# Performance work log

Measured on AMD Instinct MI355X. Metric: run time of the kernel, lower is better.

The kernel has to match this reference:

```python
import jax, jax.numpy as jnp
import numpy as np

IMAGE_SIZE = 256
VIEW_ANGLE = 30.0 * np.pi / 180.0  # NMR default viewing angle
SIGMA = 1e-2                        # softness of the differentiable coverage test
EPS = 1e-6


def setup_inputs() -> dict:
    key = jax.random.key(0)
    k1, k2, k3 = jax.random.split(key, 3)
    V, F = 502, 1000
    # normalize_vertices -> points on/near the unit sphere centered at origin
    verts = jax.random.normal(k1, (1, V, 3), dtype=jnp.float32)
    verts = verts / (jnp.linalg.norm(verts, axis=-1, keepdims=True) + EPS)
    faces = jax.random.randint(k2, (1, F, 3), 0, V, dtype=jnp.int32)
    camera_position = jnp.array([6.0, 10.0, -14.0], dtype=jnp.float32)
    # binary silhouette reference, as produced by (image.max(-1) > 0.1)
    image_ref = (jax.random.uniform(k3, (1, IMAGE_SIZE, IMAGE_SIZE)) > 0.5).astype(jnp.float32)
    return {"vertices": verts, "faces": faces, "camera_position": camera_position, "image_ref": image_ref}


def _look_at(vertices, eye):
    # camera_mode='look_at': at=origin, up=+y
    at = jnp.zeros(3, dtype=vertices.dtype)
    up = jnp.array([0.0, 1.0, 0.0], dtype=vertices.dtype)
    z = at - eye
    z = z / (jnp.linalg.norm(z) + EPS)
    x = jnp.cross(up, z)
    x = x / (jnp.linalg.norm(x) + EPS)
    y = jnp.cross(z, x)
    R = jnp.stack([x, y, z], axis=0)           # [3,3], rows are camera axes
    return jnp.einsum('bvj,ij->bvi', vertices - eye, R)  # [1,V,3]


def _render_silhouette(vertices, faces, eye):
    H = W = IMAGE_SIZE
    v = _look_at(vertices, eye)                # [1,V,3] camera space
    w = jnp.tan(jnp.asarray(VIEW_ANGLE, v.dtype))
    zc = v[..., 2]
    proj = jnp.stack([v[..., 0] / (zc * w), v[..., 1] / (zc * w)], axis=-1)  # [1,V,2] NDC xy
    fv = proj[0][faces[0]]                     # [F,3,2] projected triangle vertices
    v0, v1, v2 = fv[:, 0], fv[:, 1], fv[:, 2]

    # pixel centers in NDC, row 0 at top (y=+)
    xs = (2.0 * jnp.arange(W, dtype=v.dtype) + 1.0) / W - 1.0
    ys = 1.0 - (2.0 * jnp.arange(H, dtype=v.dtype) + 1.0) / H
    px = jnp.stack(jnp.meshgrid(xs, ys, indexing='xy'), axis=-1).reshape(-1, 2)  # [P,2]

    def edge_sdist(a, b):
        # signed distance of every pixel to line a->b, computed as px @ n^T - (a.n)
        e = b - a                                           # [F,2]
        n = jnp.stack([-e[:, 1], e[:, 0]], axis=-1)
        n = n / (jnp.linalg.norm(e, axis=-1, keepdims=True) + EPS)
        return px @ n.T - jnp.sum(a * n, axis=-1)[None, :]  # [P,F]

    # orient consistently via signed triangle area
    e01, e02 = v1 - v0, v2 - v0
    area = e01[:, 0] * e02[:, 1] - e01[:, 1] * e02[:, 0]    # [F]
    s = jnp.sign(area)[None, :]

    inv_sigma = 1.0 / SIGMA
    frag = (jax.nn.sigmoid(edge_sdist(v0, v1) * s * inv_sigma)
            * jax.nn.sigmoid(edge_sdist(v1, v2) * s * inv_sigma)
            * jax.nn.sigmoid(edge_sdist(v2, v0) * s * inv_sigma))  # [P,F] soft coverage

    sil = 1.0 - jnp.prod(1.0 - frag, axis=1)                # soft-or over faces, [P]
    return sil.reshape(1, H, W)


def reference(vertices, faces, camera_position, image_ref):
    image = _render_silhouette(vertices, faces, camera_position)  # [1,H,W]
    loss = jnp.sum((image - image_ref) ** 2)
    return loss
```

## Files before the change

kernel.cpp:

```cpp
#include <hip/hip_runtime.h>
#include <math.h>

#define IMG 256
#define NPIX (IMG*IMG)
#define SIGMA_INV 100.0f
#define EPSF 1e-6f
#define LOG2E 1.4426950408889634f
#define TANV 0.5773502691896258f
#define TSKIP 24.0f
#define FMAX 1024
#define NWAVE 8
#define NBLK (NPIX/64)

__device__ __forceinline__ float fexp2(float x) {
#if __has_builtin(__builtin_amdgcn_exp2f)
  return __builtin_amdgcn_exp2f(x);
#else
  return exp2f(x);
#endif
}
__device__ __forceinline__ float frcp(float x) {
#if __has_builtin(__builtin_amdgcn_rcpf)
  return __builtin_amdgcn_rcpf(x);
#else
  return 1.0f / x;
#endif
}
__device__ __forceinline__ float rlane(float x, int j) {
#if __has_builtin(__builtin_amdgcn_readlane)
  return __int_as_float(__builtin_amdgcn_readlane(__float_as_int(x), j));
#else
  return __shfl(x, j);
#endif
}

__device__ __forceinline__ float cross2(float ax, float ay, float bx, float by) {
#pragma clang fp contract(off)
  return ax * by - ay * bx;
}

__global__ void prep_kernel(const float* __restrict__ verts,
                            const int* __restrict__ faces,
                            const float* __restrict__ cam,
                            float4* __restrict__ fd0, float4* __restrict__ fd1,
                            float4* __restrict__ fd2, int F) {
  int f = blockIdx.x * blockDim.x + threadIdx.x;
  if (f >= F) return;
  float ex = cam[0], ey = cam[1], ez = cam[2];
  float zn = sqrtf(ex * ex + ey * ey + ez * ez) + EPSF;
  float izn = frcp(zn);
  float zx = -ex * izn, zy = -ey * izn, zz = -ez * izn;
  float xn = sqrtf(zz * zz + zx * zx) + EPSF;
  float ixn = frcp(xn);
  float xx = zz * ixn, xz = -zx * ixn;
  float yx = zy * xz;
  float yy = zz * xx - zx * xz;
  float yz = -zy * xx;

  int i0 = faces[3 * f + 0], i1 = faces[3 * f + 1], i2 = faces[3 * f + 2];
  bool deg = (i0 == i1) | (i1 == i2) | (i0 == i2);
  int vi_[3] = {i0, i1, i2};

  float pxs[3], pys[3];
#pragma unroll
  for (int k = 0; k < 3; ++k) {
    int vi = vi_[k];
    float ax = verts[3 * vi + 0] - ex;
    float ay = verts[3 * vi + 1] - ey;
    float az = verts[3 * vi + 2] - ez;
    float vx = ax * xx + az * xz;
    float vy = ax * yx + ay * yy + az * yz;
    float vz = ax * zx + ay * zy + az * zz;
    float izw = frcp(vz * TANV);
    pxs[k] = vx * izw;
    pys[k] = vy * izw;
  }
  float e01x = pxs[1] - pxs[0], e01y = pys[1] - pys[0];
  float e02x = pxs[2] - pxs[0], e02y = pys[2] - pys[0];
  float area = cross2(e01x, e01y, e02x, e02y);
  float s = deg ? 0.0f
                : ((area > 0.0f) ? 1.0f : ((area < 0.0f) ? -1.0f : 0.0f));
  float K = -s * SIGMA_INV * LOG2E;
  float4 o[3];
#pragma unroll
  for (int k = 0; k < 3; ++k) {
    int kn = (k == 2) ? 0 : k + 1;
    float dx = pxs[kn] - pxs[k], dy = pys[kn] - pys[k];
    float il = frcp(sqrtf(dx * dx + dy * dy) + EPSF);
    float nx = -dy * il, ny = dx * il;
    float c = pxs[k] * nx + pys[k] * ny;
    o[k] = make_float4(nx * K, ny * K, -c * K, 0.0f);
  }
  fd0[f] = o[0]; fd1[f] = o[1]; fd2[f] = o[2];
}

__global__ __launch_bounds__(512) void sil_kernel(
    const float4* __restrict__ fd0, const float4* __restrict__ fd1,
    const float4* __restrict__ fd2, const float* __restrict__ ref,
    float* __restrict__ bsum, int F, int fpc) {
  __shared__ float s_part[NWAVE * 64];

  int tid = threadIdx.x;
  int lane = tid & 63, w = tid >> 6;
  int bx = blockIdx.x & 31, by = blockIdx.x >> 5;
  int ix = (bx << 3) + (lane & 7);
  int iy = (by << 3) + (lane >> 3);
  float px = (2.0f * (float)ix + 1.0f) * (1.0f / IMG) - 1.0f;
  float py = 1.0f - (2.0f * (float)iy + 1.0f) * (1.0f / IMG);
  float cx = ((float)(16 * bx + 8)) * (1.0f / IMG) - 1.0f;
  float cy = 1.0f - ((float)(16 * by + 8)) * (1.0f / IMG);
  const float h = 7.0f / IMG;

  int f0 = w * fpc;
  int f1 = f0 + fpc; if (f1 > F) f1 = F;

  float acc = 1.0f;
  for (int base = f0; base < f1; base += 64) {
    int f = base + lane;
    int idx = f < F ? f : F - 1;
    float4 a0 = fd0[idx];
    float4 a1 = fd1[idx];
    float4 a2 = fd2[idx];
    float m0 = fmaf(cx, a0.x, fmaf(cy, a0.y, a0.z)) - (fabsf(a0.x) + fabsf(a0.y)) * h;
    float m1 = fmaf(cx, a1.x, fmaf(cy, a1.y, a1.z)) - (fabsf(a1.x) + fabsf(a1.y)) * h;
    float m2 = fmaf(cx, a2.x, fmaf(cy, a2.y, a2.z)) - (fabsf(a2.x) + fabsf(a2.y)) * h;
    bool rel = (f < f1) && (fmaxf(m0, fmaxf(m1, m2)) < TSKIP);
    unsigned long long mask = __ballot(rel ? 1 : 0);
    while (mask) {
      int j = __builtin_ctzll(mask);
      mask &= mask - 1;
      float b0x = rlane(a0.x, j), b0y = rlane(a0.y, j), b0z = rlane(a0.z, j);
      float b1x = rlane(a1.x, j), b1y = rlane(a1.y, j), b1z = rlane(a1.z, j);
      float b2x = rlane(a2.x, j), b2y = rlane(a2.y, j), b2z = rlane(a2.z, j);
      float t0 = fmaf(px, b0x, fmaf(py, b0y, b0z));
      float t1 = fmaf(px, b1x, fmaf(py, b1y, b1z));
      float t2 = fmaf(px, b2x, fmaf(py, b2y, b2z));
      float D = (1.0f + fexp2(t0)) * (1.0f + fexp2(t1)) * (1.0f + fexp2(t2));
      acc = fmaf(-frcp(D), acc, acc);
    }
  }

  s_part[w * 64 + lane] = acc;
  __syncthreads();

  if (w == 0) {
    float p = 1.0f;
#pragma unroll
    for (int c = 0; c < NWAVE; ++c) p *= s_part[c * 64 + lane];
    float sil = 1.0f - p;
    float d = sil - ref[iy * IMG + ix];
    float v = d * d;
#pragma unroll
    for (int off = 32; off > 0; off >>= 1) v += __shfl_down(v, off);
    if (lane == 0) bsum[blockIdx.x] = v;
  }
}

__global__ __launch_bounds__(256) void reduce_kernel(const float* __restrict__ bsum,
                                                     float* __restrict__ out) {
  int tid = threadIdx.x;
  float v = 0.0f;
  for (int i = tid; i < NBLK; i += 256) v += bsum[i];
#pragma unroll
  for (int off = 32; off > 0; off >>= 1) v += __shfl_down(v, off);
  __shared__ float red[4];
  if ((tid & 63) == 0) red[tid >> 6] = v;
  __syncthreads();
  if (tid == 0) out[0] = red[0] + red[1] + red[2] + red[3];
}

extern "C" void kernel_launch(void* const* d_in, const int* in_sizes, int n_in,
                              void* d_out, int out_size, void* d_ws, size_t ws_size,
                              hipStream_t stream) {
  const float* verts = (const float*)d_in[0];
  const int* faces = (const int*)d_in[1];
  const float* cam = (const float*)d_in[2];
  const float* imref = (const float*)d_in[3];
  int V = in_sizes[0] / 3;  (void)V;
  int F = in_sizes[1] / 3;
  float* out = (float*)d_out;

  char* ws = (char*)d_ws;
  float4* fd0 = (float4*)(ws + 0 * FMAX * 16);
  float4* fd1 = (float4*)(ws + 1 * FMAX * 16);
  float4* fd2 = (float4*)(ws + 2 * FMAX * 16);
  float* bsum = (float*)(ws + 3 * FMAX * 16);

  prep_kernel<<<(F + 255) / 256, 256, 0, stream>>>(verts, faces, cam,
                                                   fd0, fd1, fd2, F);
  int fpc = (F + NWAVE - 1) / NWAVE;
  sil_kernel<<<NBLK, 512, 0, stream>>>(fd0, fd1, fd2, imref, bsum, F, fpc);
  reduce_kernel<<<1, 256, 0, stream>>>(bsum, out);
}
```

Before: 89.16 us.

## Split faces into chunks across blocks with scrambled tile order and separate loss pass

The silhouette kernel now launches four blocks per 8x8 pixel tile, each handling a quarter of the faces, and writes per-chunk partial products to a workspace buffer. Block indices are permuted with a multiplicative hash so that heavy and light tiles spread across CUs for better load balance. A new loss kernel multiplies the four partials, computes the squared error against the reference, and reduces per block before a final reduction. This adds more parallelism and evens out work, at the cost of an extra kernel launch and roughly 1 MB of partial-product traffic.

```diff
diff --git a/kernel.cpp b/kernel.cpp
--- a/kernel.cpp
+++ b/kernel.cpp
@@ -10,7 +10,10 @@
 #define TSKIP 24.0f
 #define FMAX 1024
 #define NWAVE 8
-#define NBLK (NPIX/64)
+#define NTILE 1024
+#define NCHUNK 4
+#define NSBLK (NTILE*NCHUNK)
+#define NLBLK 128
 
 __device__ __forceinline__ float fexp2(float x) {
 #if __has_builtin(__builtin_amdgcn_exp2f)
@@ -96,13 +99,15 @@
 
 __global__ __launch_bounds__(512) void sil_kernel(
     const float4* __restrict__ fd0, const float4* __restrict__ fd1,
-    const float4* __restrict__ fd2, const float* __restrict__ ref,
-    float* __restrict__ bsum, int F, int fpc) {
+    const float4* __restrict__ fd2, float* __restrict__ part,
+    int F, int cpf, int fpw) {
   __shared__ float s_part[NWAVE * 64];
 
+  int q = (blockIdx.x * 1021) & (NSBLK - 1);
+  int tile = q >> 2, chunk = q & 3;
   int tid = threadIdx.x;
   int lane = tid & 63, w = tid >> 6;
-  int bx = blockIdx.x & 31, by = blockIdx.x >> 5;
+  int bx = tile & 31, by = tile >> 5;
   int ix = (bx << 3) + (lane & 7);
   int iy = (by << 3) + (lane >> 3);
   float px = (2.0f * (float)ix + 1.0f) * (1.0f / IMG) - 1.0f;
@@ -111,8 +116,10 @@
   float cy = 1.0f - ((float)(16 * by + 8)) * (1.0f / IMG);
   const float h = 7.0f / IMG;
 
-  int f0 = w * fpc;
-  int f1 = f0 + fpc; if (f1 > F) f1 = F;
+  int c0 = chunk * cpf;
+  int cF = c0 + cpf; if (cF > F) cF = F;
+  int f0 = c0 + w * fpw;
+  int f1 = f0 + fpw; if (f1 > cF) f1 = cF;
 
   float acc = 1.0f;
   for (int base = f0; base < f1; base += 64) {
@@ -147,26 +154,40 @@
     float p = 1.0f;
 #pragma unroll
     for (int c = 0; c < NWAVE; ++c) p *= s_part[c * 64 + lane];
-    float sil = 1.0f - p;
-    float d = sil - ref[iy * IMG + ix];
-    float v = d * d;
-#pragma unroll
-    for (int off = 32; off > 0; off >>= 1) v += __shfl_down(v, off);
-    if (lane == 0) bsum[blockIdx.x] = v;
-  }
-}
-
-__global__ __launch_bounds__(256) void reduce_kernel(const float* __restrict__ bsum,
+    part[chunk * NPIX + iy * IMG + ix] = p;
+  }
+}
+
+__global__ __launch_bounds__(512) void loss_kernel(const float* __restrict__ part,
+                                                   const float* __restrict__ ref,
+                                                   float* __restrict__ bsum) {
+  int p = blockIdx.x * 512 + threadIdx.x;
+  float a = part[p] * part[p + NPIX] * part[p + 2 * NPIX] * part[p + 3 * NPIX];
+  float d = (1.0f - a) - ref[p];
+  float v = d * d;
+#pragma unroll
+  for (int off = 32; off > 0; off >>= 1) v += __shfl_down(v, off);
+  __shared__ float red[8];
+  if ((threadIdx.x & 63) == 0) red[threadIdx.x >> 6] = v;
+  __syncthreads();
+  if (threadIdx.x == 0) {
+    float t = 0.0f;
+#pragma unroll
+    for (int c = 0; c < 8; ++c) t += red[c];
+    bsum[blockIdx.x] = t;
+  }
+}
+
+__global__ __launch_bounds__(128) void reduce_kernel(const float* __restrict__ bsum,
                                                      float* __restrict__ out) {
   int tid = threadIdx.x;
-  float v = 0.0f;
-  for (int i = tid; i < NBLK; i += 256) v += bsum[i];
+  float v = (tid < NLBLK) ? bsum[tid] : 0.0f;
 #pragma unroll
   for (int off = 32; off > 0; off >>= 1) v += __shfl_down(v, off);
-  __shared__ float red[4];
+  __shared__ float red[2];
   if ((tid & 63) == 0) red[tid >> 6] = v;
   __syncthreads();
-  if (tid == 0) out[0] = red[0] + red[1] + red[2] + red[3];
+  if (tid == 0) out[0] = red[0] + red[1];
 }
 
 extern "C" void kernel_launch(void* const* d_in, const int* in_sizes, int n_in,
@@ -184,11 +205,14 @@
   float4* fd0 = (float4*)(ws + 0 * FMAX * 16);
   float4* fd1 = (float4*)(ws + 1 * FMAX * 16);
   float4* fd2 = (float4*)(ws + 2 * FMAX * 16);
-  float* bsum = (float*)(ws + 3 * FMAX * 16);
+  float* part = (float*)(ws + 65536);
+  float* bsum = (float*)(ws + 65536 + NCHUNK * NPIX * 4);
 
   prep_kernel<<<(F + 255) / 256, 256, 0, stream>>>(verts, faces, cam,
                                                    fd0, fd1, fd2, F);
-  int fpc = (F + NWAVE - 1) / NWAVE;
-  sil_kernel<<<NBLK, 512, 0, stream>>>(fd0, fd1, fd2, imref, bsum, F, fpc);
-  reduce_kernel<<<1, 256, 0, stream>>>(bsum, out);
-}
+  int cpf = (F + NCHUNK - 1) / NCHUNK;
+  int fpw = (cpf + NWAVE - 1) / NWAVE;
+  sil_kernel<<<NSBLK, 512, 0, stream>>>(fd0, fd1, fd2, part, F, cpf, fpw);
+  loss_kernel<<<NLBLK, 512, 0, stream>>>(part, imref, bsum);
+  reduce_kernel<<<1, 128, 0, stream>>>(bsum, out);
+}
```

Measured after the change: 84.80 us. 1.05x faster.

## Split face range across blocks with atomic last-block tile and global reduction

Applied to the files above, without the earlier changes.

Each 8x8 pixel tile's faces are split across 4 blocks of 256 threads instead of one 512-thread block, with block IDs scrambled by a multiplicative hash to spread heavy tiles. Partial products go to global memory, and the last block per tile (counted with an atomic) combines them and accumulates the loss atomically. The final block writes the output, which removes the separate reduce kernel. This adds a memset, global partial traffic, atomics and fences, and makes the float summation order nondeterministic.

```diff
diff --git a/kernel.cpp b/kernel.cpp
--- a/kernel.cpp
+++ b/kernel.cpp
@@ -9,8 +9,9 @@
 #define TANV 0.5773502691896258f
 #define TSKIP 24.0f
 #define FMAX 1024
-#define NWAVE 8
-#define NBLK (NPIX/64)
+#define NCHUNK 4
+#define NTILE 1024
+#define NSBLK (NTILE*NCHUNK)
 
 __device__ __forceinline__ float fexp2(float x) {
 #if __has_builtin(__builtin_amdgcn_exp2f)
@@ -94,79 +95,84 @@
   fd0[f] = o[0]; fd1[f] = o[1]; fd2[f] = o[2];
 }
 
-__global__ __launch_bounds__(512) void sil_kernel(
+__global__ __launch_bounds__(256) void sil_kernel(
     const float4* __restrict__ fd0, const float4* __restrict__ fd1,
     const float4* __restrict__ fd2, const float* __restrict__ ref,
-    float* __restrict__ bsum, int F, int fpc) {
-  __shared__ float s_part[NWAVE * 64];
-
+    float* part, unsigned int* tile_done, float* accum,
+    unsigned int* done_tiles, float* out, int F, int cpf) {
+  __shared__ float s_part[NCHUNK * 64];
+  __shared__ unsigned int s_old;
+
+  int q = (blockIdx.x * 1637) & (NSBLK - 1);
+  int tile = q >> 2, chunk = q & 3;
   int tid = threadIdx.x;
   int lane = tid & 63, w = tid >> 6;
-  int bx = blockIdx.x & 31, by = blockIdx.x >> 5;
+  int bx = tile & 31, by = tile >> 5;
   int ix = (bx << 3) + (lane & 7);
   int iy = (by << 3) + (lane >> 3);
+  int pix = iy * IMG + ix;
   float px = (2.0f * (float)ix + 1.0f) * (1.0f / IMG) - 1.0f;
   float py = 1.0f - (2.0f * (float)iy + 1.0f) * (1.0f / IMG);
   float cx = ((float)(16 * bx + 8)) * (1.0f / IMG) - 1.0f;
   float cy = 1.0f - ((float)(16 * by + 8)) * (1.0f / IMG);
   const float h = 7.0f / IMG;
 
-  int f0 = w * fpc;
-  int f1 = f0 + fpc; if (f1 > F) f1 = F;
+  int r = w * 64 + lane;
+  int f = chunk * cpf + r;
+  int idx = (f < F) ? f : F - 1;
+  float4 a0 = fd0[idx];
+  float4 a1 = fd1[idx];
+  float4 a2 = fd2[idx];
+  float m0 = fmaf(cx, a0.x, fmaf(cy, a0.y, a0.z)) - (fabsf(a0.x) + fabsf(a0.y)) * h;
+  float m1 = fmaf(cx, a1.x, fmaf(cy, a1.y, a1.z)) - (fabsf(a1.x) + fabsf(a1.y)) * h;
+  float m2 = fmaf(cx, a2.x, fmaf(cy, a2.y, a2.z)) - (fabsf(a2.x) + fabsf(a2.y)) * h;
+  bool rel = (r < cpf) && (f < F) && (fmaxf(m0, fmaxf(m1, m2)) < TSKIP);
+  unsigned long long mask = __ballot(rel ? 1 : 0);
 
   float acc = 1.0f;
-  for (int base = f0; base < f1; base += 64) {
-    int f = base + lane;
-    int idx = f < F ? f : F - 1;
-    float4 a0 = fd0[idx];
-    float4 a1 = fd1[idx];
-    float4 a2 = fd2[idx];
-    float m0 = fmaf(cx, a0.x, fmaf(cy, a0.y, a0.z)) - (fabsf(a0.x) + fabsf(a0.y)) * h;
-    float m1 = fmaf(cx, a1.x, fmaf(cy, a1.y, a1.z)) - (fabsf(a1.x) + fabsf(a1.y)) * h;
-    float m2 = fmaf(cx, a2.x, fmaf(cy, a2.y, a2.z)) - (fabsf(a2.x) + fabsf(a2.y)) * h;
-    bool rel = (f < f1) && (fmaxf(m0, fmaxf(m1, m2)) < TSKIP);
-    unsigned long long mask = __ballot(rel ? 1 : 0);
-    while (mask) {
-      int j = __builtin_ctzll(mask);
-      mask &= mask - 1;
-      float b0x = rlane(a0.x, j), b0y = rlane(a0.y, j), b0z = rlane(a0.z, j);
-      float b1x = rlane(a1.x, j), b1y = rlane(a1.y, j), b1z = rlane(a1.z, j);
-      float b2x = rlane(a2.x, j), b2y = rlane(a2.y, j), b2z = rlane(a2.z, j);
-      float t0 = fmaf(px, b0x, fmaf(py, b0y, b0z));
-      float t1 = fmaf(px, b1x, fmaf(py, b1y, b1z));
-      float t2 = fmaf(px, b2x, fmaf(py, b2y, b2z));
-      float D = (1.0f + fexp2(t0)) * (1.0f + fexp2(t1)) * (1.0f + fexp2(t2));
-      acc = fmaf(-frcp(D), acc, acc);
-    }
+  while (mask) {
+    int j = __builtin_ctzll(mask);
+    mask &= mask - 1;
+    float b0x = rlane(a0.x, j), b0y = rlane(a0.y, j), b0z = rlane(a0.z, j);
+    float b1x = rlane(a1.x, j), b1y = rlane(a1.y, j), b1z = rlane(a1.z, j);
+    float b2x = rlane(a2.x, j), b2y = rlane(a2.y, j), b2z = rlane(a2.z, j);
+    float t0 = fmaf(px, b0x, fmaf(py, b0y, b0z));
+    float t1 = fmaf(px, b1x, fmaf(py, b1y, b1z));
+    float t2 = fmaf(px, b2x, fmaf(py, b2y, b2z));
+    float D = (1.0f + fexp2(t0)) * (1.0f + fexp2(t1)) * (1.0f + fexp2(t2));
+    acc = fmaf(-frcp(D), acc, acc);
   }
 
   s_part[w * 64 + lane] = acc;
   __syncthreads();
 
   if (w == 0) {
-    float p = 1.0f;
-#pragma unroll
-    for (int c = 0; c < NWAVE; ++c) p *= s_part[c * 64 + lane];
-    float sil = 1.0f - p;
-    float d = sil - ref[iy * IMG + ix];
+    float p = s_part[lane] * s_part[64 + lane] *
+              s_part[128 + lane] * s_part[192 + lane];
+    part[chunk * NPIX + pix] = p;
+    __threadfence();
+    if (lane == 0) s_old = atomicAdd(&tile_done[tile], 1u);
+  }
+  __syncthreads();
+
+  if (w == 0 && s_old == NCHUNK - 1) {
+    __threadfence();
+    float a = part[pix] * part[pix + NPIX] *
+              part[pix + 2 * NPIX] * part[pix + 3 * NPIX];
+    float d = (1.0f - a) - ref[pix];
     float v = d * d;
 #pragma unroll
     for (int off = 32; off > 0; off >>= 1) v += __shfl_down(v, off);
-    if (lane == 0) bsum[blockIdx.x] = v;
-  }
-}
-
-__global__ __launch_bounds__(256) void reduce_kernel(const float* __restrict__ bsum,
-                                                     float* __restrict__ out) {
-  int tid = threadIdx.x;
-  float v = 0.0f;
-  for (int i = tid; i < NBLK; i += 256) v += bsum[i];
-#pragma unroll
-  for (int off = 32; off > 0; off >>= 1) v += __shfl_down(v, off);
-  __shared__ float red[4];
-  if ((tid & 63) == 0) red[tid >> 6] = v;
-  __syncthreads();
-  if (tid == 0) out[0] = red[0] + red[1] + red[2] + red[3];
+    if (lane == 0) {
+      atomicAdd(accum, v);
+      __threadfence();
+      unsigned int t = atomicAdd(done_tiles, 1u);
+      if (t == NTILE - 1) {
+        __threadfence();
+        out[0] = atomicAdd(accum, 0.0f);
+      }
+    }
+  }
 }
 
 extern "C" void kernel_launch(void* const* d_in, const int* in_sizes, int n_in,
@@ -181,14 +187,19 @@
   float* out = (float*)d_out;
 
   char* ws = (char*)d_ws;
-  float4* fd0 = (float4*)(ws + 0 * FMAX * 16);
-  float4* fd1 = (float4*)(ws + 1 * FMAX * 16);
-  float4* fd2 = (float4*)(ws + 2 * FMAX * 16);
-  float* bsum = (float*)(ws + 3 * FMAX * 16);
-
+  float* accum = (float*)ws;
+  unsigned int* done_tiles = (unsigned int*)(ws + 4);
+  unsigned int* tile_done = (unsigned int*)(ws + 8);
+  float4* fd0 = (float4*)(ws + 8192);
+  float4* fd1 = (float4*)(ws + 8192 + FMAX * 16);
+  float4* fd2 = (float4*)(ws + 8192 + 2 * FMAX * 16);
+  float* part = (float*)(ws + 65536);
+
+  hipMemsetAsync(ws, 0, 8 + NTILE * 4, stream);
   prep_kernel<<<(F + 255) / 256, 256, 0, stream>>>(verts, faces, cam,
                                                    fd0, fd1, fd2, F);
-  int fpc = (F + NWAVE - 1) / NWAVE;
-  sil_kernel<<<NBLK, 512, 0, stream>>>(fd0, fd1, fd2, imref, bsum, F, fpc);
-  reduce_kernel<<<1, 256, 0, stream>>>(bsum, out);
-}
+  int cpf = (F + NCHUNK - 1) / NCHUNK;
+  sil_kernel<<<NSBLK, 256, 0, stream>>>(fd0, fd1, fd2, imref, part,
+                                        tile_done, accum, done_tiles, out,
+                                        F, cpf);
+}
```

Result: slower. 208.9 us (+134.3%).
